# Kernel tuning notes

Hardware: AMD Instinct MI355X
Metric: run time of the kernel (lower is better)

The kernel has to match this reference:

```python
import jax, jax.numpy as jnp
import numpy as np

N, E, D, H, OUT = 50000, 262144, 128, 256, 1
NUM_EXPERTS, TOP_K = 4, 1


def _mlp(x, w1, b1, w2, b2):
    return jnp.maximum(x @ w1 + b1, 0.0) @ w2 + b2


def setup_inputs() -> dict:
    key = jax.random.key(0)
    ks = jax.random.split(key, 16)
    def lin(k, fan_in, fan_out):
        bound = 1.0 / np.sqrt(fan_in)
        return jax.random.uniform(k, (fan_in, fan_out), jnp.float32, -bound, bound)
    return {
        "z": jax.random.normal(ks[0], (N, D), jnp.float32),
        "u": jax.random.randint(ks[1], (E,), 0, N, jnp.int64),
        "v": jax.random.randint(ks[2], (E,), 0, N, jnp.int64),
        "gate_w": lin(ks[3], 4 * D, NUM_EXPERTS),
        "gate_b": jnp.zeros((NUM_EXPERTS,), jnp.float32),
        "cat_w1": lin(ks[4], 2 * D, H), "cat_b1": jnp.zeros((H,), jnp.float32),
        "cat_w2": lin(ks[5], H, OUT), "cat_b2": jnp.zeros((OUT,), jnp.float32),
        "dist_w1": lin(ks[6], D, H), "dist_b1": jnp.zeros((H,), jnp.float32),
        "dist_w2": lin(ks[7], H, OUT), "dist_b2": jnp.zeros((OUT,), jnp.float32),
        "mul_w1": lin(ks[8], D, H), "mul_b1": jnp.zeros((H,), jnp.float32),
        "mul_w2": lin(ks[9], H, OUT), "mul_b2": jnp.zeros((OUT,), jnp.float32),
        "all_w1": lin(ks[10], 4 * D, H), "all_b1": jnp.zeros((H,), jnp.float32),
        "all_w2": lin(ks[11], H, OUT), "all_b2": jnp.zeros((OUT,), jnp.float32),
    }


def reference(z, u, v, gate_w, gate_b,
              cat_w1, cat_b1, cat_w2, cat_b2,
              dist_w1, dist_b1, dist_w2, dist_b2,
              mul_w1, mul_b1, mul_w2, mul_b2,
              all_w1, all_b1, all_w2, all_b2):
    z_u = z[u]                      # [E, D]
    z_v = z[v]                      # [E, D]
    z_cat = jnp.concatenate([z_u, z_v], axis=-1)        # [E, 2D]
    z_diff = jnp.abs(z_u - z_v)                         # [E, D]
    z_mul = z_u * z_v                                   # [E, D]
    edge_feat = jnp.concatenate([z_cat, z_diff, z_mul], axis=-1)  # [E, 4D]

    s1 = _mlp(z_cat, cat_w1, cat_b1, cat_w2, cat_b2)
    s2 = _mlp(z_diff, dist_w1, dist_b1, dist_w2, dist_b2)
    s3 = _mlp(z_mul, mul_w1, mul_b1, mul_w2, mul_b2)
    s4 = _mlp(edge_feat, all_w1, all_b1, all_w2, all_b2)
    scores = jnp.stack([s1, s2, s3, s4], axis=1)        # [E, 4, OUT]

    gate_logits = edge_feat @ gate_w + gate_b           # [E, 4]
    gate_probs = jax.nn.softmax(gate_logits, axis=-1)

    # top_k=1 with straight-through estimator (forward value == hard gate)
    topk_vals, topk_idx = jax.lax.top_k(gate_probs, TOP_K)
    hard_gate = jax.nn.one_hot(topk_idx[:, 0], NUM_EXPERTS, dtype=gate_probs.dtype) * topk_vals[:, :1]
    gate_st = hard_gate + gate_probs - jax.lax.stop_gradient(gate_probs)

    out = jnp.einsum("ek,eko->eo", gate_st, scores)     # [E, OUT]
    # dropout is identity in eval mode
    avg_expert_usage = gate_probs.mean(axis=0)
    aux_loss = (avg_expert_usage ** 2).sum() * NUM_EXPERTS
    return out, aux_loss
```

## Files before the change

kernel.cpp:

```cpp
#include <hip/hip_runtime.h>
#include <hip/hip_bf16.h>
#include <math.h>

#define N_NODES 50000
#define E_EDGES 262144
#define D_FEAT  128
#define H_HID   256
#define NEXP    4

typedef __attribute__((ext_vector_type(8))) short  short8;
typedef __attribute__((ext_vector_type(4))) float  floatx4;

#define W1B_OFF0 0
#define W1B_OFF1 65536
#define W1B_OFF2 98304
#define W1B_OFF3 131072

__device__ __forceinline__ unsigned short f2bf(float f) {
    __hip_bfloat16 h = __float2bfloat16(f);
    return *reinterpret_cast<unsigned short*>(&h);
}

__global__ __launch_bounds__(256) void prep_kernel(
    const float* __restrict__ cw1, const float* __restrict__ dw1,
    const float* __restrict__ mw1, const float* __restrict__ aw1,
    unsigned short* __restrict__ w1b,
    const float* __restrict__ z, const float* __restrict__ gw,
    double* __restrict__ nodeTab, double* __restrict__ gwd)
{
    int bx  = blockIdx.x;
    int tid = threadIdx.x;

    if (bx < 1024) {
        int r = bx, n = tid;
        const float* src; int k, off;
        if (r < 256)      { src = cw1; k = r;       off = W1B_OFF0; }
        else if (r < 384) { src = dw1; k = r - 256; off = W1B_OFF1; }
        else if (r < 512) { src = mw1; k = r - 384; off = W1B_OFF2; }
        else              { src = aw1; k = r - 512; off = W1B_OFF3; }
        w1b[off + (((k >> 3) * 256 + n) << 3) + (k & 7)] = f2bf(src[k * 256 + n]);
        return;
    }

    int n = (bx - 1024) * 256 + tid;
    if (n < 128) {
        #pragma unroll
        for (int k = 0; k < 4; ++k) {
            gwd[n * 8 + k]     = (double)gw[4 * (256 + n) + k];
            gwd[n * 8 + 4 + k] = (double)gw[4 * (384 + n) + k];
        }
    }
    if (n >= N_NODES) return;

    const float4* zr = (const float4*)(z + (long)n * D_FEAT);
    double u0 = 0, u1 = 0, u2 = 0, u3 = 0;
    double v0 = 0, v1 = 0, v2 = 0, v3 = 0;
    for (int d4 = 0; d4 < D_FEAT / 4; ++d4) {
        float4 a = zr[d4];
        float av[4] = {a.x, a.y, a.z, a.w};
        #pragma unroll
        for (int j = 0; j < 4; ++j) {
            int d = d4 * 4 + j;
            const float4 g0 = *(const float4*)(gw + 4 * d);
            const float4 g1 = *(const float4*)(gw + 4 * (128 + d));
            double ad = (double)av[j];
            u0 += ad * (double)g0.x; u1 += ad * (double)g0.y;
            u2 += ad * (double)g0.z; u3 += ad * (double)g0.w;
            v0 += ad * (double)g1.x; v1 += ad * (double)g1.y;
            v2 += ad * (double)g1.z; v3 += ad * (double)g1.w;
        }
    }
    double* o = nodeTab + (long)n * 8;
    o[0] = u0; o[1] = u1; o[2] = u2; o[3] = u3;
    o[4] = v0; o[5] = v1; o[6] = v2; o[7] = v3;
}

__global__ __launch_bounds__(256) void gate_kernel(
    const float* __restrict__ z, const int* __restrict__ u, const int* __restrict__ v,
    const double* __restrict__ nodeTab, const double* __restrict__ gwd,
    const float* __restrict__ gb,
    float* __restrict__ probsum, unsigned* __restrict__ gcount,
    int* __restrict__ lists, float* __restrict__ pval)
{
    int tid  = threadIdx.x;
    int lane = tid & 63;
    int half = tid & 1;
    int e    = blockIdx.x * 128 + (tid >> 1);

    __shared__ double s_gwd[1024];
    __shared__ float  s_ps[4];
    __shared__ int    s_cnt[4];
    __shared__ int    s_base[4];

    #pragma unroll
    for (int i = 0; i < 4; ++i)
        s_gwd[tid + i * 256] = gwd[tid + i * 256];
    if (tid < 4) { s_ps[tid] = 0.0f; s_cnt[tid] = 0; }
    __syncthreads();

    int ue = u[e], ve = v[e];
    const float4* zu4 = (const float4*)(z + (long)ue * D_FEAT) + half * 16;
    const float4* zv4 = (const float4*)(z + (long)ve * D_FEAT) + half * 16;
    const double* grb = s_gwd + (half << 9);

    double la0 = 0, la1 = 0, la2 = 0, la3 = 0;
    double lm0 = 0, lm1 = 0, lm2 = 0, lm3 = 0;

    #pragma unroll 4
    for (int d4 = 0; d4 < 16; ++d4) {
        float4 a = zu4[d4];
        float4 b = zv4[d4];
        float av[4] = {a.x, a.y, a.z, a.w};
        float bv[4] = {b.x, b.y, b.z, b.w};
        #pragma unroll
        for (int j = 0; j < 4; ++j) {
            double ad = (double)fabsf(av[j] - bv[j]);
            double m  = (double)(av[j] * bv[j]);
            const double* gr = grb + (d4 * 4 + j) * 8;
            la0 += ad * gr[0]; lm0 += m * gr[4];
            la1 += ad * gr[1]; lm1 += m * gr[5];
            la2 += ad * gr[2]; lm2 += m * gr[6];
            la3 += ad * gr[3]; lm3 += m * gr[7];
        }
    }

    double l0 = la0 + lm0, l1 = la1 + lm1, l2 = la2 + lm2, l3 = la3 + lm3;
    if (half == 0) {
        const double* nu = nodeTab + (long)ue * 8;
        const double* nv = nodeTab + (long)ve * 8;
        l0 += (double)gb[0] + nu[0] + nv[4];
        l1 += (double)gb[1] + nu[1] + nv[5];
        l2 += (double)gb[2] + nu[2] + nv[6];
        l3 += (double)gb[3] + nu[3] + nv[7];
    }
    l0 += __shfl_xor(l0, 1);
    l1 += __shfl_xor(l1, 1);
    l2 += __shfl_xor(l2, 1);
    l3 += __shfl_xor(l3, 1);

    int sel = 0;
    double lb = l0;
    if (l1 > lb) { lb = l1; sel = 1; }
    if (l2 > lb) { lb = l2; sel = 2; }
    if (l3 > lb) { lb = l3; sel = 3; }

    float e0 = expf((float)(l0 - lb));
    float e1 = expf((float)(l1 - lb));
    float e2 = expf((float)(l2 - lb));
    float e3 = expf((float)(l3 - lb));
    float s   = e0 + e1 + e2 + e3;
    float inv = 1.0f / s;
    float p[4];
    p[0] = e0 * inv; p[1] = e1 * inv; p[2] = e2 * inv; p[3] = e3 * inv;
    float best = p[sel];

    float q0 = half ? 0.0f : p[0];
    float q1 = half ? 0.0f : p[1];
    float q2 = half ? 0.0f : p[2];
    float q3 = half ? 0.0f : p[3];
    #pragma unroll
    for (int off = 32; off > 0; off >>= 1) {
        q0 += __shfl_down(q0, off);
        q1 += __shfl_down(q1, off);
        q2 += __shfl_down(q2, off);
        q3 += __shfl_down(q3, off);
    }
    if (lane == 0) {
        atomicAdd(&s_ps[0], q0); atomicAdd(&s_ps[1], q1);
        atomicAdd(&s_ps[2], q2); atomicAdd(&s_ps[3], q3);
    }

    const unsigned long long EV = 0x5555555555555555ull;
    unsigned long long lt = (lane == 0) ? 0ull : ((~0ull) >> (64 - lane));
    int mywb = 0, myrank = 0;
    #pragma unroll
    for (int k = 0; k < 4; ++k) {
        unsigned long long mask = __ballot(sel == k) & EV;
        if (mask) {
            int leader = (int)__ffsll((unsigned long long)mask) - 1;
            int wb = 0;
            if (lane == leader) wb = atomicAdd(&s_cnt[k], (int)__popcll(mask));
            wb = __shfl(wb, leader);
            if (half == 0 && sel == k) { mywb = wb; myrank = (int)__popcll(mask & lt); }
        }
    }
    __syncthreads();

    if (tid < 4) {
        s_base[tid] = (int)atomicAdd(&gcount[tid], (unsigned)s_cnt[tid]);
        atomicAdd(&probsum[tid], s_ps[tid]);
    }
    __syncthreads();

    if (half == 0) {
        int pos = s_base[sel] + mywb + myrank;
        lists[sel * E_EDGES + pos] = e;
        pval[e] = best;
    }
}

#define FPAD 40
#define PCHUNK 4

__device__ __forceinline__ float4 edge_feat4(int ex, const float* zu, const float* zv, int fg)
{
    if (ex == 0) {
        return (fg < 128) ? *(const float4*)(zu + fg)
                          : *(const float4*)(zv + fg - 128);
    } else if (ex == 1) {
        float4 a = *(const float4*)(zu + fg);
        float4 b = *(const float4*)(zv + fg);
        return make_float4(fabsf(a.x - b.x), fabsf(a.y - b.y),
                           fabsf(a.z - b.z), fabsf(a.w - b.w));
    } else if (ex == 2) {
        float4 a = *(const float4*)(zu + fg);
        float4 b = *(const float4*)(zv + fg);
        return make_float4(a.x * b.x, a.y * b.y, a.z * b.z, a.w * b.w);
    } else {
        if (fg < 128) {
            return *(const float4*)(zu + fg);
        } else if (fg < 256) {
            return *(const float4*)(zv + fg - 128);
        } else if (fg < 384) {
            float4 a = *(const float4*)(zu + fg - 256);
            float4 b = *(const float4*)(zv + fg - 256);
            return make_float4(fabsf(a.x - b.x), fabsf(a.y - b.y),
                               fabsf(a.z - b.z), fabsf(a.w - b.w));
        } else {
            float4 a = *(const float4*)(zu + fg - 384);
            float4 b = *(const float4*)(zv + fg - 384);
            return make_float4(a.x * b.x, a.y * b.y, a.z * b.z, a.w * b.w);
        }
    }
}

__global__ __launch_bounds__(256) void expert_kernel(
    const float* __restrict__ z, const int* __restrict__ u, const int* __restrict__ v,
    const unsigned short* __restrict__ w1b,
    const float* __restrict__ cb1, const float* __restrict__ cw2, const float* __restrict__ cb2,
    const float* __restrict__ db1, const float* __restrict__ dw2, const float* __restrict__ db2,
    const float* __restrict__ mb1, const float* __restrict__ mw2, const float* __restrict__ mb2,
    const float* __restrict__ ab1, const float* __restrict__ aw2, const float* __restrict__ ab2,
    const unsigned* __restrict__ gcount, const int* __restrict__ lists,
    const float* __restrict__ pval, const float* __restrict__ probsum,
    float* __restrict__ out)
{
    int tid = threadIdx.x;

    if (blockIdx.x == 0 && blockIdx.y == 0 && tid == 0) {
        float a = 0.0f;
        #pragma unroll
        for (int k = 0; k < 4; ++k) {
            float mean = probsum[k] * (1.0f / (float)E_EDGES);
            a += mean * mean;
        }
        out[E_EDGES] = a * (float)NEXP;
    }

    int ex = blockIdx.y;
    const float *b1, *w2, *b2;
    int F, w1off;
    if (ex == 0)      { b1 = cb1; w2 = cw2; b2 = cb2; F = 256; w1off = W1B_OFF0; }
    else if (ex == 1) { b1 = db1; w2 = dw2; b2 = db2; F = 128; w1off = W1B_OFF1; }
    else if (ex == 2) { b1 = mb1; w2 = mw2; b2 = mb2; F = 128; w1off = W1B_OFF2; }
    else              { b1 = ab1; w2 = aw2; b2 = ab2; F = 512; w1off = W1B_OFF3; }

    unsigned cnt  = gcount[ex];
    unsigned tile = blockIdx.x * 32u;
    if (tile >= cnt) return;
    int nm = (int)min(32u, cnt - tile);

    __shared__ unsigned short featA[PCHUNK][32][FPAD];
    __shared__ int   s_e[32], s_u[32], s_v[32];
    __shared__ float s_pv[32];
    __shared__ float red[4][32];

    int wave = tid >> 6;
    int lane = tid & 63;
    int colA = lane & 15;
    int quad = lane >> 4;

    if (tid < 32) {
        int m = tid;
        int src = (m < nm) ? (int)(tile + m) : (int)tile;
        int e = lists[ex * E_EDGES + src];
        s_e[m] = e; s_u[m] = u[e]; s_v[m] = v[e]; s_pv[m] = pval[e];
    }
    __syncthreads();

    const short8* wB = (const short8*)(w1b + w1off);

    floatx4 acc[2][4];
    #pragma unroll
    for (int t = 0; t < 2; ++t)
        #pragma unroll
        for (int j = 0; j < 4; ++j)
            acc[t][j] = (floatx4)(0.0f);

    int fm = tid >> 3;
    int fk = (tid & 7) << 2;
    int nc = F >> 5;
    const float* zu = z + (long)s_u[fm] * D_FEAT;
    const float* zv = z + (long)s_v[fm] * D_FEAT;
    int nb = wave * 64 + colA;

    for (int c0 = 0; c0 < nc; c0 += PCHUNK) {
        int cend = min(PCHUNK, nc - c0);
        if (c0) __syncthreads();

        for (int cc = 0; cc < cend; ++cc) {
            int fg = (c0 + cc) * 32 + fk;
            float4 val = edge_feat4(ex, zu, zv, fg);
            ushort4 pk;
            pk.x = f2bf(val.x); pk.y = f2bf(val.y);
            pk.z = f2bf(val.z); pk.w = f2bf(val.w);
            *(ushort4*)(&featA[cc][fm][fk]) = pk;
        }
        __syncthreads();

        for (int cc = 0; cc < cend; ++cc) {
            int g = (c0 + cc) * 4 + quad;
            short8 bf0 = wB[g * 256 + nb +  0];
            short8 bf1 = wB[g * 256 + nb + 16];
            short8 bf2 = wB[g * 256 + nb + 32];
            short8 bf3 = wB[g * 256 + nb + 48];

            short8 a0 = *(const short8*)(&featA[cc][colA][quad * 8]);
            short8 a1 = *(const short8*)(&featA[cc][16 + colA][quad * 8]);

            acc[0][0] = __builtin_amdgcn_mfma_f32_16x16x32_bf16(a0, bf0, acc[0][0], 0, 0, 0);
            acc[1][0] = __builtin_amdgcn_mfma_f32_16x16x32_bf16(a1, bf0, acc[1][0], 0, 0, 0);
            acc[0][1] = __builtin_amdgcn_mfma_f32_16x16x32_bf16(a0, bf1, acc[0][1], 0, 0, 0);
            acc[1][1] = __builtin_amdgcn_mfma_f32_16x16x32_bf16(a1, bf1, acc[1][1], 0, 0, 0);
            acc[0][2] = __builtin_amdgcn_mfma_f32_16x16x32_bf16(a0, bf2, acc[0][2], 0, 0, 0);
            acc[1][2] = __builtin_amdgcn_mfma_f32_16x16x32_bf16(a1, bf2, acc[1][2], 0, 0, 0);
            acc[0][3] = __builtin_amdgcn_mfma_f32_16x16x32_bf16(a0, bf3, acc[0][3], 0, 0, 0);
            acc[1][3] = __builtin_amdgcn_mfma_f32_16x16x32_bf16(a1, bf3, acc[1][3], 0, 0, 0);
        }
    }

    float b1v[4], w2v[4];
    #pragma unroll
    for (int j = 0; j < 4; ++j) {
        int h = wave * 64 + j * 16 + colA;
        b1v[j] = b1[h];
        w2v[j] = w2[h];
    }

    #pragma unroll
    for (int t = 0; t < 2; ++t) {
        #pragma unroll
        for (int r = 0; r < 4; ++r) {
            float s = 0.0f;
            #pragma unroll
            for (int j = 0; j < 4; ++j) {
                float h = acc[t][j][r] + b1v[j];
                s += fmaxf(h, 0.0f) * w2v[j];
            }
            s += __shfl_xor(s, 1);
            s += __shfl_xor(s, 2);
            s += __shfl_xor(s, 4);
            s += __shfl_xor(s, 8);
            if (colA == 0) {
                int m = 16 * t + quad * 4 + r;
                red[wave][m] = s;
            }
        }
    }
    __syncthreads();

    if (tid < 32) {
        int m = tid;
        if (m < nm) {
            float sc = red[0][m] + red[1][m] + red[2][m] + red[3][m] + b2[0];
            out[s_e[m]] = s_pv[m] * sc;
        }
    }
}

extern "C" void kernel_launch(void* const* d_in, const int* in_sizes, int n_in,
                              void* d_out, int out_size, void* d_ws, size_t ws_size,
                              hipStream_t stream)
{
    const float* z   = (const float*)d_in[0];
    const int*   u   = (const int*)d_in[1];
    const int*   v   = (const int*)d_in[2];
    const float* gw  = (const float*)d_in[3];
    const float* gb  = (const float*)d_in[4];
    const float* cw1 = (const float*)d_in[5];
    const float* cb1 = (const float*)d_in[6];
    const float* cw2 = (const float*)d_in[7];
    const float* cb2 = (const float*)d_in[8];
    const float* dw1 = (const float*)d_in[9];
    const float* db1 = (const float*)d_in[10];
    const float* dw2 = (const float*)d_in[11];
    const float* db2 = (const float*)d_in[12];
    const float* mw1 = (const float*)d_in[13];
    const float* mb1 = (const float*)d_in[14];
    const float* mw2 = (const float*)d_in[15];
    const float* mb2 = (const float*)d_in[16];
    const float* aw1 = (const float*)d_in[17];
    const float* ab1 = (const float*)d_in[18];
    const float* aw2 = (const float*)d_in[19];
    const float* ab2 = (const float*)d_in[20];

    float* out = (float*)d_out;
    char*  ws  = (char*)d_ws;

    float*          probsum = (float*)ws;
    unsigned*       gcount  = (unsigned*)(ws + 16);
    int*            lists   = (int*)(ws + 32);
    float*          pval    = (float*)(ws + 32 + 16ll * E_EDGES);
    unsigned short* w1b     = (unsigned short*)(ws + 32 + 20ll * E_EDGES);
    double*         gwd     = (double*)(ws + 32 + 20ll * E_EDGES + 524288);
    double*         nodeTab = (double*)(ws + 32 + 20ll * E_EDGES + 524288 + 8192);

    hipMemsetAsync(d_ws, 0, 32, stream);

    prep_kernel<<<1024 + (N_NODES + 255) / 256, 256, 0, stream>>>(
        cw1, dw1, mw1, aw1, w1b, z, gw, nodeTab, gwd);

    gate_kernel<<<E_EDGES / 128, 256, 0, stream>>>(z, u, v, nodeTab, gwd, gb,
                                                   probsum, gcount, lists, pval);

    dim3 g2(E_EDGES / 32, 4);
    expert_kernel<<<g2, 256, 0, stream>>>(z, u, v, w1b,
                                          cb1, cw2, cb2,
                                          db1, dw2, db2,
                                          mb1, mw2, mb2,
                                          ab1, aw2, ab2,
                                          gcount, lists, pval, probsum, out);
}
```

Before: 293.8 us.

## Double-buffer edge feature staging in LDS to overlap gathers with MFMA

Replaces the single-buffered chunk loop with a two-stage ping-pong LDS buffer. The next chunk of gathered edge features is loaded and converted while the MFMA work runs on the current chunk, which removes one barrier per pass. The chunk size drops from 4 to 2 and the buffer count doubles, so LDS use stays the same while the number of passes and barriers per tile goes up. It assumes nc is divisible by PCHUNK, which holds for F of 128, 256 and 512.

Result: no change. 294.4 us (+0.2%).

```diff
diff --git a/kernel.cpp b/kernel.cpp
--- a/kernel.cpp
+++ b/kernel.cpp
@@ -200,7 +200,7 @@
 }
 
 #define FPAD 40
-#define PCHUNK 4
+#define PCHUNK 2
 
 __device__ __forceinline__ float4 edge_feat4(int ex, const float* zu, const float* zv, int fg)
 {
@@ -270,7 +270,7 @@
     if (tile >= cnt) return;
     int nm = (int)min(32u, cnt - tile);
 
-    __shared__ unsigned short featA[PCHUNK][32][FPAD];
+    __shared__ unsigned short featA[2][PCHUNK][32][FPAD];
     __shared__ int   s_e[32], s_u[32], s_v[32];
     __shared__ float s_pv[32];
     __shared__ float red[4][32];
@@ -300,33 +300,44 @@
     int fm = tid >> 3;
     int fk = (tid & 7) << 2;
     int nc = F >> 5;
+    int nPass = nc / PCHUNK;
     const float* zu = z + (long)s_u[fm] * D_FEAT;
     const float* zv = z + (long)s_v[fm] * D_FEAT;
     int nb = wave * 64 + colA;
 
-    for (int c0 = 0; c0 < nc; c0 += PCHUNK) {
-        int cend = min(PCHUNK, nc - c0);
-        if (c0) __syncthreads();
-
-        for (int cc = 0; cc < cend; ++cc) {
-            int fg = (c0 + cc) * 32 + fk;
-            float4 val = edge_feat4(ex, zu, zv, fg);
-            ushort4 pk;
-            pk.x = f2bf(val.x); pk.y = f2bf(val.y);
-            pk.z = f2bf(val.z); pk.w = f2bf(val.w);
-            *(ushort4*)(&featA[cc][fm][fk]) = pk;
-        }
-        __syncthreads();
-
-        for (int cc = 0; cc < cend; ++cc) {
-            int g = (c0 + cc) * 4 + quad;
+    #pragma unroll
+    for (int cc = 0; cc < PCHUNK; ++cc) {
+        float4 val = edge_feat4(ex, zu, zv, cc * 32 + fk);
+        ushort4 pk;
+        pk.x = f2bf(val.x); pk.y = f2bf(val.y);
+        pk.z = f2bf(val.z); pk.w = f2bf(val.w);
+        *(ushort4*)(&featA[0][cc][fm][fk]) = pk;
+    }
+    __syncthreads();
+
+    int cur = 0;
+    for (int p = 0; p < nPass; ++p) {
+        if (p + 1 < nPass) {
+            #pragma unroll
+            for (int cc = 0; cc < PCHUNK; ++cc) {
+                float4 val = edge_feat4(ex, zu, zv, ((p + 1) * PCHUNK + cc) * 32 + fk);
+                ushort4 pk;
+                pk.x = f2bf(val.x); pk.y = f2bf(val.y);
+                pk.z = f2bf(val.z); pk.w = f2bf(val.w);
+                *(ushort4*)(&featA[cur ^ 1][cc][fm][fk]) = pk;
+            }
+        }
+
+        #pragma unroll
+        for (int cc = 0; cc < PCHUNK; ++cc) {
+            int g = (p * PCHUNK + cc) * 4 + quad;
             short8 bf0 = wB[g * 256 + nb +  0];
             short8 bf1 = wB[g * 256 + nb + 16];
             short8 bf2 = wB[g * 256 + nb + 32];
             short8 bf3 = wB[g * 256 + nb + 48];
 
-            short8 a0 = *(const short8*)(&featA[cc][colA][quad * 8]);
-            short8 a1 = *(const short8*)(&featA[cc][16 + colA][quad * 8]);
+            short8 a0 = *(const short8*)(&featA[cur][cc][colA][quad * 8]);
+            short8 a1 = *(const short8*)(&featA[cur][cc][16 + colA][quad * 8]);
 
             acc[0][0] = __builtin_amdgcn_mfma_f32_16x16x32_bf16(a0, bf0, acc[0][0], 0, 0, 0);
             acc[1][0] = __builtin_amdgcn_mfma_f32_16x16x32_bf16(a1, bf0, acc[1][0], 0, 0, 0);
@@ -337,6 +348,9 @@
             acc[0][3] = __builtin_amdgcn_mfma_f32_16x16x32_bf16(a0, bf3, acc[0][3], 0, 0, 0);
             acc[1][3] = __builtin_amdgcn_mfma_f32_16x16x32_bf16(a1, bf3, acc[1][3], 0, 0, 0);
         }
+
+        __syncthreads();
+        cur ^= 1;
     }
 
     float b1v[4], w2v[4];
```

## Stage raw gathered node rows in LDS and build expert features on the fly

Applied to the files above, without the earlier changes.

Instead of repeatedly gathering z rows from global memory per feature chunk and writing bf16 feature tiles to LDS with barriers between chunks, each block now loads the 32 u-rows and 32 v-rows once into a padded fp32 LDS buffer. Each wave then builds its MFMA A-operands directly from LDS (concat, abs-diff or product) inside a barrier-free K loop. This removes redundant global gathers for the 'all' expert and the per-chunk syncs, at the cost of more LDS (64x132 floats) and duplicated feature arithmetic across waves.

After: 296.8 us. About the same (+1.0%).

```diff
diff --git a/kernel.cpp b/kernel.cpp
--- a/kernel.cpp
+++ b/kernel.cpp
@@ -199,39 +199,36 @@
     }
 }
 
-#define FPAD 40
-#define PCHUNK 4
-
-__device__ __forceinline__ float4 edge_feat4(int ex, const float* zu, const float* zv, int fg)
+#define ZPAD 132
+
+__device__ __forceinline__ short8 build8(const float* pu, const float* pv, int mode)
 {
-    if (ex == 0) {
-        return (fg < 128) ? *(const float4*)(zu + fg)
-                          : *(const float4*)(zv + fg - 128);
-    } else if (ex == 1) {
-        float4 a = *(const float4*)(zu + fg);
-        float4 b = *(const float4*)(zv + fg);
-        return make_float4(fabsf(a.x - b.x), fabsf(a.y - b.y),
-                           fabsf(a.z - b.z), fabsf(a.w - b.w));
-    } else if (ex == 2) {
-        float4 a = *(const float4*)(zu + fg);
-        float4 b = *(const float4*)(zv + fg);
-        return make_float4(a.x * b.x, a.y * b.y, a.z * b.z, a.w * b.w);
+    float o[8];
+    if (mode == 0) {
+        float4 x0 = *(const float4*)pu, x1 = *(const float4*)(pu + 4);
+        o[0]=x0.x; o[1]=x0.y; o[2]=x0.z; o[3]=x0.w;
+        o[4]=x1.x; o[5]=x1.y; o[6]=x1.z; o[7]=x1.w;
+    } else if (mode == 1) {
+        float4 y0 = *(const float4*)pv, y1 = *(const float4*)(pv + 4);
+        o[0]=y0.x; o[1]=y0.y; o[2]=y0.z; o[3]=y0.w;
+        o[4]=y1.x; o[5]=y1.y; o[6]=y1.z; o[7]=y1.w;
+    } else if (mode == 2) {
+        float4 x0 = *(const float4*)pu, x1 = *(const float4*)(pu + 4);
+        float4 y0 = *(const float4*)pv, y1 = *(const float4*)(pv + 4);
+        o[0]=fabsf(x0.x-y0.x); o[1]=fabsf(x0.y-y0.y); o[2]=fabsf(x0.z-y0.z); o[3]=fabsf(x0.w-y0.w);
+        o[4]=fabsf(x1.x-y1.x); o[5]=fabsf(x1.y-y1.y); o[6]=fabsf(x1.z-y1.z); o[7]=fabsf(x1.w-y1.w);
     } else {
-        if (fg < 128) {
-            return *(const float4*)(zu + fg);
-        } else if (fg < 256) {
-            return *(const float4*)(zv + fg - 128);
-        } else if (fg < 384) {
-            float4 a = *(const float4*)(zu + fg - 256);
-            float4 b = *(const float4*)(zv + fg - 256);
-            return make_float4(fabsf(a.x - b.x), fabsf(a.y - b.y),
-                               fabsf(a.z - b.z), fabsf(a.w - b.w));
-        } else {
-            float4 a = *(const float4*)(zu + fg - 384);
-            float4 b = *(const float4*)(zv + fg - 384);
-            return make_float4(a.x * b.x, a.y * b.y, a.z * b.z, a.w * b.w);
-        }
-    }
+        float4 x0 = *(const float4*)pu, x1 = *(const float4*)(pu + 4);
+        float4 y0 = *(const float4*)pv, y1 = *(const float4*)(pv + 4);
+        o[0]=x0.x*y0.x; o[1]=x0.y*y0.y; o[2]=x0.z*y0.z; o[3]=x0.w*y0.w;
+        o[4]=x1.x*y1.x; o[5]=x1.y*y1.y; o[6]=x1.z*y1.z; o[7]=x1.w*y1.w;
+    }
+    short8 r;
+    r[0]=(short)f2bf(o[0]); r[1]=(short)f2bf(o[1]);
+    r[2]=(short)f2bf(o[2]); r[3]=(short)f2bf(o[3]);
+    r[4]=(short)f2bf(o[4]); r[5]=(short)f2bf(o[5]);
+    r[6]=(short)f2bf(o[6]); r[7]=(short)f2bf(o[7]);
+    return r;
 }
 
 __global__ __launch_bounds__(256) void expert_kernel(
@@ -270,7 +267,7 @@
     if (tile >= cnt) return;
     int nm = (int)min(32u, cnt - tile);
 
-    __shared__ unsigned short featA[PCHUNK][32][FPAD];
+    __shared__ float s_zr[64][ZPAD];
     __shared__ int   s_e[32], s_u[32], s_v[32];
     __shared__ float s_pv[32];
     __shared__ float red[4][32];
@@ -288,6 +285,17 @@
     }
     __syncthreads();
 
+    {
+        int r  = tid >> 2;
+        int cs = (tid & 3) << 5;
+        int node = (r < 32) ? s_u[r] : s_v[r - 32];
+        const float4* src = (const float4*)(z + (long)node * D_FEAT + cs);
+        float4* dst = (float4*)(&s_zr[r][cs]);
+        #pragma unroll
+        for (int i = 0; i < 8; ++i) dst[i] = src[i];
+    }
+    __syncthreads();
+
     const short8* wB = (const short8*)(w1b + w1off);
 
     floatx4 acc[2][4];
@@ -297,46 +305,37 @@
         for (int j = 0; j < 4; ++j)
             acc[t][j] = (floatx4)(0.0f);
 
-    int fm = tid >> 3;
-    int fk = (tid & 7) << 2;
     int nc = F >> 5;
-    const float* zu = z + (long)s_u[fm] * D_FEAT;
-    const float* zv = z + (long)s_v[fm] * D_FEAT;
     int nb = wave * 64 + colA;
 
-    for (int c0 = 0; c0 < nc; c0 += PCHUNK) {
-        int cend = min(PCHUNK, nc - c0);
-        if (c0) __syncthreads();
-
-        for (int cc = 0; cc < cend; ++cc) {
-            int fg = (c0 + cc) * 32 + fk;
-            float4 val = edge_feat4(ex, zu, zv, fg);
-            ushort4 pk;
-            pk.x = f2bf(val.x); pk.y = f2bf(val.y);
-            pk.z = f2bf(val.z); pk.w = f2bf(val.w);
-            *(ushort4*)(&featA[cc][fm][fk]) = pk;
-        }
-        __syncthreads();
-
-        for (int cc = 0; cc < cend; ++cc) {
-            int g = (c0 + cc) * 4 + quad;
-            short8 bf0 = wB[g * 256 + nb +  0];
-            short8 bf1 = wB[g * 256 + nb + 16];
-            short8 bf2 = wB[g * 256 + nb + 32];
-            short8 bf3 = wB[g * 256 + nb + 48];
-
-            short8 a0 = *(const short8*)(&featA[cc][colA][quad * 8]);
-            short8 a1 = *(const short8*)(&featA[cc][16 + colA][quad * 8]);
-
-            acc[0][0] = __builtin_amdgcn_mfma_f32_16x16x32_bf16(a0, bf0, acc[0][0], 0, 0, 0);
-            acc[1][0] = __builtin_amdgcn_mfma_f32_16x16x32_bf16(a1, bf0, acc[1][0], 0, 0, 0);
-            acc[0][1] = __builtin_amdgcn_mfma_f32_16x16x32_bf16(a0, bf1, acc[0][1], 0, 0, 0);
-            acc[1][1] = __builtin_amdgcn_mfma_f32_16x16x32_bf16(a1, bf1, acc[1][1], 0, 0, 0);
-            acc[0][2] = __builtin_amdgcn_mfma_f32_16x16x32_bf16(a0, bf2, acc[0][2], 0, 0, 0);
-            acc[1][2] = __builtin_amdgcn_mfma_f32_16x16x32_bf16(a1, bf2, acc[1][2], 0, 0, 0);
-            acc[0][3] = __builtin_amdgcn_mfma_f32_16x16x32_bf16(a0, bf3, acc[0][3], 0, 0, 0);
-            acc[1][3] = __builtin_amdgcn_mfma_f32_16x16x32_bf16(a1, bf3, acc[1][3], 0, 0, 0);
-        }
+    for (int c = 0; c < nc; ++c) {
+        int kbase = c << 5;
+        int mode, roff;
+        if (ex == 1)      { mode = 2; roff = kbase; }
+        else if (ex == 2) { mode = 3; roff = kbase; }
+        else {
+            mode = kbase >> 7;
+            roff = kbase & 127;
+        }
+        int kl = roff + (quad << 3);
+
+        short8 a0 = build8(&s_zr[colA][kl],      &s_zr[32 + colA][kl],      mode);
+        short8 a1 = build8(&s_zr[16 + colA][kl], &s_zr[48 + colA][kl],      mode);
+
+        int g = (c << 2) + quad;
+        short8 bf0 = wB[g * 256 + nb +  0];
+        short8 bf1 = wB[g * 256 + nb + 16];
+        short8 bf2 = wB[g * 256 + nb + 32];
+        short8 bf3 = wB[g * 256 + nb + 48];
+
+        acc[0][0] = __builtin_amdgcn_mfma_f32_16x16x32_bf16(a0, bf0, acc[0][0], 0, 0, 0);
+        acc[1][0] = __builtin_amdgcn_mfma_f32_16x16x32_bf16(a1, bf0, acc[1][0], 0, 0, 0);
+        acc[0][1] = __builtin_amdgcn_mfma_f32_16x16x32_bf16(a0, bf1, acc[0][1], 0, 0, 0);
+        acc[1][1] = __builtin_amdgcn_mfma_f32_16x16x32_bf16(a1, bf1, acc[1][1], 0, 0, 0);
+        acc[0][2] = __builtin_amdgcn_mfma_f32_16x16x32_bf16(a0, bf2, acc[0][2], 0, 0, 0);
+        acc[1][2] = __builtin_amdgcn_mfma_f32_16x16x32_bf16(a1, bf2, acc[1][2], 0, 0, 0);
+        acc[0][3] = __builtin_amdgcn_mfma_f32_16x16x32_bf16(a0, bf3, acc[0][3], 0, 0, 0);
+        acc[1][3] = __builtin_amdgcn_mfma_f32_16x16x32_bf16(a1, bf3, acc[1][3], 0, 0, 0);
     }
 
     float b1v[4], w2v[4];
```
